# Kernel tuning notes

Hardware: AMD Instinct MI355X
Metric: run time of the kernel (lower is better)

## Reference

```python
import jax, jax.numpy as jnp
import numpy as np

D_MODEL = 1024
N_HEADS = 16
HEAD_DIM = D_MODEL // N_HEADS  # 64
D_STATE = 128
D_FF = 4 * D_MODEL
EPS = 1e-6


def rmsnorm(x, w):
    xf = x.astype(jnp.float32)
    var = jnp.mean(xf * xf, axis=-1, keepdims=True)
    return (w * (x * jax.lax.rsqrt(var + EPS))).astype(x.dtype)


def setup_inputs() -> dict:
    key = jax.random.key(0)
    ks = jax.random.split(key, 24)
    B, S = 2, 2048
    inv = lambda n: 1.0 / np.sqrt(n)
    inp = {
        "x": jax.random.normal(ks[0], (B, S, D_MODEL), jnp.float32),
        "attn_mask": jnp.triu(jnp.ones((S, S), jnp.bool_), k=1),  # True = masked (causal)
        "norm1_w": jnp.ones((D_MODEL,), jnp.float32),
        "norm2_w": jnp.ones((D_MODEL,), jnp.float32),
        "norm3_w": jnp.ones((D_MODEL,), jnp.float32),
        "mlpn_w": jnp.ones((D_MODEL,), jnp.float32),
        # projections stored [in, out]; torch Linear y = x @ W.T
        "wq": jax.random.normal(ks[1], (D_MODEL, D_MODEL), jnp.float32) * inv(D_MODEL),
        "wk": jax.random.normal(ks[2], (D_MODEL, D_MODEL), jnp.float32) * inv(D_MODEL),
        "wv": jax.random.normal(ks[3], (D_MODEL, D_MODEL), jnp.float32) * inv(D_MODEL),
        "wo": jax.random.normal(ks[4], (D_MODEL, D_MODEL), jnp.float32) * inv(D_MODEL),
        "qs_w1": jax.random.normal(ks[5], (HEAD_DIM, D_STATE), jnp.float32) * inv(HEAD_DIM),
        "qs_b1": jnp.zeros((D_STATE,), jnp.float32),
        "qs_w2": jax.random.normal(ks[6], (D_STATE, HEAD_DIM), jnp.float32) * inv(D_STATE),
        "qs_b2": jnp.zeros((HEAD_DIM,), jnp.float32),
        "ks_w1": jax.random.normal(ks[7], (HEAD_DIM, D_STATE), jnp.float32) * inv(HEAD_DIM),
        "ks_b1": jnp.zeros((D_STATE,), jnp.float32),
        "ks_w2": jax.random.normal(ks[8], (D_STATE, HEAD_DIM), jnp.float32) * inv(D_STATE),
        "ks_b2": jnp.zeros((HEAD_DIM,), jnp.float32),
        "fc1_w": jax.random.normal(ks[9], (D_MODEL, D_FF), jnp.float32) * inv(D_MODEL),
        "fc1_b": jnp.zeros((D_FF,), jnp.float32),
        "fc2_w": jax.random.normal(ks[10], (D_FF, D_MODEL), jnp.float32) * inv(D_FF),
        "fc2_b": jnp.zeros((D_MODEL,), jnp.float32),
        "gate_w": jax.random.normal(ks[11], (D_MODEL, D_FF), jnp.float32) * inv(D_MODEL),
        "gate_b": jnp.zeros((D_FF,), jnp.float32),
    }
    return inp


def _attention(h, attn_mask, wq, wk, wv, wo,
               qs_w1, qs_b1, qs_w2, qs_b2, ks_w1, ks_b1, ks_w2, ks_b2):
    B, S, _ = h.shape
    q = (h @ wq).reshape(B, S, N_HEADS, HEAD_DIM)
    k = (h @ wk).reshape(B, S, N_HEADS, HEAD_DIM)
    v = (h @ wv).reshape(B, S, N_HEADS, HEAD_DIM)
    # per-head SiLU-MLP residual transform; weights shared across heads -> vectorized
    q = jax.nn.silu(q @ qs_w1 + qs_b1) @ qs_w2 + qs_b2 + q
    k = jax.nn.silu(k @ ks_w1 + ks_b1) @ ks_w2 + ks_b2 + k
    scale = HEAD_DIM ** -0.5
    scores = jnp.einsum('bqhd,bkhd->bhqk', q, k) * scale
    scores = jnp.where(attn_mask[None, None, :, :], -jnp.inf, scores)
    attn = jax.nn.softmax(scores, axis=-1)
    out = jnp.einsum('bhqk,bkhd->bqhd', attn, v).reshape(B, S, D_MODEL)
    return out @ wo


def reference(x, attn_mask, norm1_w, norm2_w, norm3_w, mlpn_w,
              wq, wk, wv, wo,
              qs_w1, qs_b1, qs_w2, qs_b2, ks_w1, ks_b1, ks_w2, ks_b2,
              fc1_w, fc1_b, fc2_w, fc2_b, gate_w, gate_b):
    # Mamba2Block fallback (mamba_ssm unavailable) is the identity on its input,
    # so each mamba stage is: x = x + RMSNorm(x). Dropout is inference identity.
    x = x + rmsnorm(x, norm1_w)
    x = x + rmsnorm(x, norm2_w)
    h = rmsnorm(x, norm3_w)
    x = x + _attention(h, attn_mask, wq, wk, wv, wo,
                       qs_w1, qs_b1, qs_w2, qs_b2, ks_w1, ks_b1, ks_w2, ks_b2)
    hn = rmsnorm(x, mlpn_w)
    gate = jax.nn.silu(hn @ gate_w + gate_b)
    y = gate * (hn @ fc1_w + fc1_b)
    x = x + (y @ fc2_w + fc2_b)
    return x
```

## Files before the change

### kernel.cpp

```cpp
#include <hip/hip_runtime.h>

typedef unsigned short u16;
typedef unsigned int u32;
typedef __bf16 bf16x8 __attribute__((ext_vector_type(8)));
typedef float f32x4 __attribute__((ext_vector_type(4)));

#define D_MODEL 1024
#define SEQ 2048
#define NB 2
#define NH 16
#define HD 64
#define NTOK (NB * SEQ)
#define NTH (NTOK * NH)
#define LDQ 3072

__device__ __forceinline__ float bf2f(u16 v) { return __uint_as_float(((u32)v) << 16); }
__device__ __forceinline__ u16 f2bf(float f) {
    u32 x = __float_as_uint(f);
    x += 0x7fffu + ((x >> 16) & 1u);
    return (u16)(x >> 16);
}
__device__ __forceinline__ u32 cvtpk(float lo, float hi) {
    u32 r;
    asm("v_cvt_pk_bf16_f32 %0, %1, %2" : "=v"(r) : "v"(lo), "v"(hi));
    return r;
}
__device__ __forceinline__ void unp4(uint2 v, float* f) {
    f[0] = __uint_as_float(v.x << 16);
    f[1] = __uint_as_float(v.x & 0xffff0000u);
    f[2] = __uint_as_float(v.y << 16);
    f[3] = __uint_as_float(v.y & 0xffff0000u);
}

__device__ __forceinline__ void gload_lds(const u16* g, u16* l) {
    __builtin_amdgcn_global_load_lds((__attribute__((address_space(1))) u32*)g,
                                     (__attribute__((address_space(3))) u32*)l, 16, 0, 0);
}

__global__ void detect_kernel(const u32* __restrict__ n1w, int* __restrict__ flag) {
    if (threadIdx.x == 0 && blockIdx.x == 0) flag[0] = (n1w[0] == 0x3F800000u) ? 1 : 0;
}

struct CJobs { const void* in[12]; u16* out[12]; int n[12]; };

__global__ __launch_bounds__(256) void convmulti_kernel(CJobs jobs, const int* __restrict__ flag) {
    const bool f32 = flag[0] != 0;
    const int j = blockIdx.y;
    const int n = jobs.n[j];
    const float* fb = (const float*)jobs.in[j];
    const u16* ib = (const u16*)jobs.in[j];
    u16* ob = jobs.out[j];
    int i = (blockIdx.x * 256 + threadIdx.x) * 8;
    const int str = gridDim.x * 256 * 8;
    for (; i < n; i += str) {
        u16 v[8];
        if (f32) {
#pragma unroll
            for (int t = 0; t < 8; ++t) v[t] = f2bf(fb[i + t]);
        } else {
            *(uint4*)v = *(const uint4*)(ib + i);
        }
        *(uint4*)(ob + i) = *(uint4*)v;
    }
}

struct TJobs { const void* in[4]; u16* out[4]; int kd[4]; int nd[4]; };

__global__ __launch_bounds__(256) void tconvm_kernel(TJobs jobs, const int* __restrict__ flag) {
    __shared__ float tile[32][33];
    const int j = blockIdx.z;
    const int Kd = jobs.kd[j], Nd = jobs.nd[j];
    const int k0 = blockIdx.y * 32, n0 = blockIdx.x * 32;
    if (k0 >= Kd || n0 >= Nd) return;
    const bool f32 = flag[0] != 0;
    const void* in = jobs.in[j];
    u16* out = jobs.out[j];
    const int tx = threadIdx.x & 31, ty = threadIdx.x >> 5;
#pragma unroll
    for (int kk = ty; kk < 32; kk += 8) {
        const size_t sidx = (size_t)(k0 + kk) * Nd + n0 + tx;
        tile[kk][tx] = f32 ? ((const float*)in)[sidx] : bf2f(((const u16*)in)[sidx]);
    }
    __syncthreads();
#pragma unroll
    for (int nn = ty; nn < 32; nn += 8)
        out[(size_t)(n0 + nn) * Kd + k0 + tx] = f2bf(tile[tx][nn]);
}

__device__ __forceinline__ float block_sum(float v, float* red, int tid) {
#pragma unroll
    for (int off = 32; off; off >>= 1) v += __shfl_xor(v, off, 64);
    if ((tid & 63) == 0) red[tid >> 6] = v;
    __syncthreads();
    v = red[0] + red[1] + red[2] + red[3];
    __syncthreads();
    return v;
}

__global__ __launch_bounds__(256) void norm3_kernel(const u16* __restrict__ X,
                                                    const u16* __restrict__ w1,
                                                    const u16* __restrict__ w2,
                                                    const u16* __restrict__ w3,
                                                    float* __restrict__ X2,
                                                    u16* __restrict__ H) {
    __shared__ float red[4];
    const int row = blockIdx.x, tid = threadIdx.x;
    const int c = tid * 4;
    const size_t base = (size_t)row * D_MODEL + c;
    float x[4], w[4];
    unp4(*reinterpret_cast<const uint2*>(X + base), x);

    float ss = x[0] * x[0] + x[1] * x[1] + x[2] * x[2] + x[3] * x[3];
    ss = block_sum(ss, red, tid);
    float r = rsqrtf(ss * (1.f / D_MODEL) + 1e-6f);
    unp4(*reinterpret_cast<const uint2*>(w1 + c), w);
#pragma unroll
    for (int i = 0; i < 4; ++i) x[i] = x[i] + w[i] * x[i] * r;

    ss = x[0] * x[0] + x[1] * x[1] + x[2] * x[2] + x[3] * x[3];
    ss = block_sum(ss, red, tid);
    r = rsqrtf(ss * (1.f / D_MODEL) + 1e-6f);
    unp4(*reinterpret_cast<const uint2*>(w2 + c), w);
#pragma unroll
    for (int i = 0; i < 4; ++i) x[i] = x[i] + w[i] * x[i] * r;

    *reinterpret_cast<float4*>(X2 + base) = make_float4(x[0], x[1], x[2], x[3]);

    ss = x[0] * x[0] + x[1] * x[1] + x[2] * x[2] + x[3] * x[3];
    ss = block_sum(ss, red, tid);
    r = rsqrtf(ss * (1.f / D_MODEL) + 1e-6f);
    unp4(*reinterpret_cast<const uint2*>(w3 + c), w);
    uint2 hv;
    hv.x = (u32)f2bf(w[0] * x[0] * r) | ((u32)f2bf(w[1] * x[1] * r) << 16);
    hv.y = (u32)f2bf(w[2] * x[2] * r) | ((u32)f2bf(w[3] * x[3] * r) << 16);
    *reinterpret_cast<uint2*>(H + base) = hv;
}

__global__ __launch_bounds__(256) void hn_norm_kernel(const float* __restrict__ X3,
                                                      const u16* __restrict__ w,
                                                      u16* __restrict__ HN) {
    __shared__ float red[4];
    const int row = blockIdx.x, tid = threadIdx.x;
    const int c = tid * 4;
    const size_t base = (size_t)row * D_MODEL + c;
    float4 xv = *reinterpret_cast<const float4*>(X3 + base);
    float x[4] = {xv.x, xv.y, xv.z, xv.w};
    float ss = x[0] * x[0] + x[1] * x[1] + x[2] * x[2] + x[3] * x[3];
    ss = block_sum(ss, red, tid);
    float r = rsqrtf(ss * (1.f / D_MODEL) + 1e-6f);
    float w4[4];
    unp4(*reinterpret_cast<const uint2*>(w + c), w4);
    uint2 hv;
    hv.x = (u32)f2bf(w4[0] * x[0] * r) | ((u32)f2bf(w4[1] * x[1] * r) << 16);
    hv.y = (u32)f2bf(w4[2] * x[2] * r) | ((u32)f2bf(w4[3] * x[3] * r) << 16);
    *reinterpret_cast<uint2*>(HN + base) = hv;
}

__global__ __launch_bounds__(256, 4) void mgemm_kernel(const u16* __restrict__ A,
                                                       const u16* __restrict__ Bt,
                                                       const u16* __restrict__ bias,
                                                       const float* __restrict__ resf,
                                                       const u16* __restrict__ mul,
                                                       void* __restrict__ Cout,
                                                       int M, int N, int K, int act, int outf32,
                                                       const int* __restrict__ oflag) {
    __shared__ u16 As[128 * 64];
    __shared__ u16 Bs[128 * 64];
    const int tid = threadIdx.x;
    const int w = tid >> 6, lane = tid & 63;
    const int quad = lane >> 4, l16 = lane & 15;
    const int m0 = blockIdx.y * 128, n0 = blockIdx.x * 128;
    const int wr = (w >> 1) * 64, wc = (w & 1) * 64;

    const int srow = lane >> 3;
    const int scol = ((lane & 7) ^ srow) * 8;
    const u16* Ar = A + (size_t)(m0 + w * 32 + srow) * K + scol;
    const u16* Br = Bt + (size_t)(n0 + w * 32 + srow) * K + scol;
    const int sl0 = l16 & 7;

    f32x4 acc[4][4] = {};

    for (int k0 = 0; k0 < K; k0 += 64) {
#pragma unroll
        for (int i = 0; i < 4; ++i) {
            gload_lds(Ar + (size_t)(i * 8) * K + k0, &As[(w * 32 + i * 8) * 64]);
            gload_lds(Br + (size_t)(i * 8) * K + k0, &Bs[(w * 32 + i * 8) * 64]);
        }
        __syncthreads();
#pragma unroll
        for (int kk = 0; kk < 2; ++kk) {
            const int slot = ((kk * 4 + quad) ^ sl0) * 8;
            bf16x8 a[4], b[4];
#pragma unroll
            for (int i = 0; i < 4; ++i)
                a[i] = *(const bf16x8*)&As[(wr + i * 16 + l16) * 64 + slot];
#pragma unroll
            for (int j = 0; j < 4; ++j)
                b[j] = *(const bf16x8*)&Bs[(wc + j * 16 + l16) * 64 + slot];
#pragma unroll
            for (int i = 0; i < 4; ++i)
#pragma unroll
                for (int j = 0; j < 4; ++j)
                    acc[i][j] = __builtin_amdgcn_mfma_f32_16x16x32_bf16(a[i], b[j], acc[i][j], 0, 0, 0);
        }
        __syncthreads();
    }

    const bool of32 = oflag ? (oflag[0] != 0) : (outf32 != 0);
#pragma unroll
    for (int j = 0; j < 4; ++j) {
        const int col = n0 + wc + j * 16 + l16;
        const float bv = bias ? bf2f(bias[col]) : 0.f;
#pragma unroll
        for (int i = 0; i < 4; ++i) {
            const int rowb = m0 + wr + i * 16 + quad * 4;
#pragma unroll
            for (int r = 0; r < 4; ++r) {
                float v = acc[i][j][r] + bv;
                const size_t idx = (size_t)(rowb + r) * N + col;
                if (act) v = v / (1.f + __expf(-v));
                if (mul) v *= bf2f(mul[idx]);
                if (resf) v += resf[idx];
                if (of32)
                    ((float*)Cout)[idx] = v;
                else
                    ((u16*)Cout)[idx] = f2bf(v);
            }
        }
    }
}

__global__ __launch_bounds__(256, 2) void gatefc1_kernel(const u16* __restrict__ A,
                                                         const u16* __restrict__ Bg,
                                                         const u16* __restrict__ Bf,
                                                         const u16* __restrict__ gbias,
                                                         const u16* __restrict__ fbias,
                                                         u16* __restrict__ G1) {
    const int N = 4096, K = 1024;
    __shared__ u16 As[128 * 64];
    __shared__ u16 Bgs[128 * 64];
    __shared__ u16 Bfs[128 * 64];
    const int tid = threadIdx.x;
    const int w = tid >> 6, lane = tid & 63;
    const int quad = lane >> 4, l16 = lane & 15;
    const int m0 = blockIdx.y * 128, n0 = blockIdx.x * 128;
    const int wr = (w >> 1) * 64, wc = (w & 1) * 64;

    const int srow = lane >> 3;
    const int scol = ((lane & 7) ^ srow) * 8;
    const u16* Ar = A + (size_t)(m0 + w * 32 + srow) * K + scol;
    const u16* Bgr = Bg + (size_t)(n0 + w * 32 + srow) * K + scol;
    const u16* Bfr = Bf + (size_t)(n0 + w * 32 + srow) * K + scol;
    const int sl0 = l16 & 7;

    f32x4 accg[4][4] = {};
    f32x4 accf[4][4] = {};

    for (int k0 = 0; k0 < K; k0 += 64) {
#pragma unroll
        for (int i = 0; i < 4; ++i) {
            gload_lds(Ar + (size_t)(i * 8) * K + k0, &As[(w * 32 + i * 8) * 64]);
            gload_lds(Bgr + (size_t)(i * 8) * K + k0, &Bgs[(w * 32 + i * 8) * 64]);
            gload_lds(Bfr + (size_t)(i * 8) * K + k0, &Bfs[(w * 32 + i * 8) * 64]);
        }
        __syncthreads();
#pragma unroll
        for (int kk = 0; kk < 2; ++kk) {
            const int slot = ((kk * 4 + quad) ^ sl0) * 8;
            bf16x8 a[4], b[4];
#pragma unroll
            for (int i = 0; i < 4; ++i)
                a[i] = *(const bf16x8*)&As[(wr + i * 16 + l16) * 64 + slot];
#pragma unroll
            for (int j = 0; j < 4; ++j)
                b[j] = *(const bf16x8*)&Bgs[(wc + j * 16 + l16) * 64 + slot];
#pragma unroll
            for (int i = 0; i < 4; ++i)
#pragma unroll
                for (int j = 0; j < 4; ++j)
                    accg[i][j] = __builtin_amdgcn_mfma_f32_16x16x32_bf16(a[i], b[j], accg[i][j], 0, 0, 0);
#pragma unroll
            for (int j = 0; j < 4; ++j)
                b[j] = *(const bf16x8*)&Bfs[(wc + j * 16 + l16) * 64 + slot];
#pragma unroll
            for (int i = 0; i < 4; ++i)
#pragma unroll
                for (int j = 0; j < 4; ++j)
                    accf[i][j] = __builtin_amdgcn_mfma_f32_16x16x32_bf16(a[i], b[j], accf[i][j], 0, 0, 0);
        }
        __syncthreads();
    }

#pragma unroll
    for (int j = 0; j < 4; ++j) {
        const int col = n0 + wc + j * 16 + l16;
        const float gb = bf2f(gbias[col]);
        const float fb = bf2f(fbias[col]);
#pragma unroll
        for (int i = 0; i < 4; ++i) {
            const int rowb = m0 + wr + i * 16 + quad * 4;
#pragma unroll
            for (int r = 0; r < 4; ++r) {
                float g = accg[i][j][r] + gb;
                g = g / (1.f + __expf(-g));
                const float f = accf[i][j][r] + fb;
                G1[(size_t)(rowb + r) * N + col] = f2bf(g * f);
            }
        }
    }
}

__global__ __launch_bounds__(256) void mgemm64_kernel(const u16* __restrict__ A,
                                                      const u16* __restrict__ Bt,
                                                      const u16* __restrict__ bias,
                                                      const float* __restrict__ resf,
                                                      const u16* __restrict__ mul,
                                                      void* __restrict__ Cout,
                                                      int M, int N, int K, int act, int outf32,
                                                      const int* __restrict__ oflag) {
    __shared__ u16 As[3][64 * 64];
    __shared__ u16 Bs[3][128 * 64];
    const int tid = threadIdx.x;
    const int w = tid >> 6, lane = tid & 63;
    const int quad = lane >> 4, l16 = lane & 15;
    const int m0 = blockIdx.y * 64, n0 = blockIdx.x * 128;
    const int wr = (w >> 1) * 32, wc = (w & 1) * 64;

    const int srow = lane >> 3;
    const int scol = ((lane & 7) ^ srow) * 8;
    const u16* Ar = A + (size_t)(m0 + w * 16 + srow) * K + scol;
    const u16* Br = Bt + (size_t)(n0 + w * 32 + srow) * K + scol;
    const int sl0 = l16 & 7;

    f32x4 acc[2][4] = {};
    const int nt = K >> 6;

    auto STAGE = [&](int t, int buf) {
        const int k0 = t * 64;
#pragma unroll
        for (int i = 0; i < 2; ++i)
            gload_lds(Ar + (size_t)(i * 8) * K + k0, &As[buf][(w * 16 + i * 8) * 64]);
#pragma unroll
        for (int i = 0; i < 4; ++i)
            gload_lds(Br + (size_t)(i * 8) * K + k0, &Bs[buf][(w * 32 + i * 8) * 64]);
    };
    auto COMPUTE = [&](int buf) {
#pragma unroll
        for (int kk = 0; kk < 2; ++kk) {
            const int slot = ((kk * 4 + quad) ^ sl0) * 8;
            bf16x8 a[2], b[4];
#pragma unroll
            for (int i = 0; i < 2; ++i)
                a[i] = *(const bf16x8*)&As[buf][(wr + i * 16 + l16) * 64 + slot];
#pragma unroll
            for (int j = 0; j < 4; ++j)
                b[j] = *(const bf16x8*)&Bs[buf][(wc + j * 16 + l16) * 64 + slot];
#pragma unroll
            for (int i = 0; i < 2; ++i)
#pragma unroll
                for (int j = 0; j < 4; ++j)
                    acc[i][j] = __builtin_amdgcn_mfma_f32_16x16x32_bf16(a[i], b[j], acc[i][j], 0, 0, 0);
        }
    };

    STAGE(0, 0);
    STAGE(1, 1);
    int cb = 0, sb = 2;
    for (int t = 0; t < nt - 2; ++t) {
        STAGE(t + 2, sb);
        asm volatile("s_waitcnt vmcnt(12)" ::: "memory");
        __builtin_amdgcn_sched_barrier(0);
        __builtin_amdgcn_s_barrier();
        COMPUTE(cb);
        __builtin_amdgcn_s_barrier();
        cb = (cb + 1 == 3) ? 0 : cb + 1;
        sb = (sb + 1 == 3) ? 0 : sb + 1;
    }
    asm volatile("s_waitcnt vmcnt(6)" ::: "memory");
    __builtin_amdgcn_sched_barrier(0);
    __builtin_amdgcn_s_barrier();
    COMPUTE(cb);
    __builtin_amdgcn_s_barrier();
    cb = (cb + 1 == 3) ? 0 : cb + 1;
    asm volatile("s_waitcnt vmcnt(0)" ::: "memory");
    __builtin_amdgcn_sched_barrier(0);
    __builtin_amdgcn_s_barrier();
    COMPUTE(cb);

    const bool of32 = oflag ? (oflag[0] != 0) : (outf32 != 0);
#pragma unroll
    for (int j = 0; j < 4; ++j) {
        const int col = n0 + wc + j * 16 + l16;
        const float bv = bias ? bf2f(bias[col]) : 0.f;
#pragma unroll
        for (int i = 0; i < 2; ++i) {
            const int rowb = m0 + wr + i * 16 + quad * 4;
#pragma unroll
            for (int r = 0; r < 4; ++r) {
                float v = acc[i][j][r] + bv;
                const size_t idx = (size_t)(rowb + r) * N + col;
                if (act) v = v / (1.f + __expf(-v));
                if (mul) v *= bf2f(mul[idx]);
                if (resf) v += resf[idx];
                if (of32)
                    ((float*)Cout)[idx] = v;
                else
                    ((u16*)Cout)[idx] = f2bf(v);
            }
        }
    }
}

__global__ __launch_bounds__(256) void headmlp2_kernel(
    u16* __restrict__ QKV,
    const u16* __restrict__ W1tq, const u16* __restrict__ B1q,
    const u16* __restrict__ W2tq, const u16* __restrict__ B2q,
    const u16* __restrict__ W1tk, const u16* __restrict__ B1k,
    const u16* __restrict__ W2tk, const u16* __restrict__ B2k) {
    __shared__ u16 w1s[128 * 64];
    __shared__ u16 w2s[64 * 128];
    __shared__ u16 Ps[4][16 * 136];
    const int tid = threadIdx.x;
    const bool isk = blockIdx.y != 0;
    u16* base = QKV + (isk ? 1024 : 0);
    const u16* W1t = isk ? W1tk : W1tq;
    const u16* B1 = isk ? B1k : B1q;
    const u16* W2t = isk ? W2tk : W2tq;
    const u16* B2 = isk ? B2k : B2q;

    for (int i = tid * 8; i < 8192; i += 2048) {
        *(uint4*)&w1s[i] = *(const uint4*)&W1t[i];
        *(uint4*)&w2s[i] = *(const uint4*)&W2t[i];
    }
    __syncthreads();

    const int w = tid >> 6, lane = tid & 63;
    const int l16 = lane & 15, quad = lane >> 4;
    const int tok0 = blockIdx.x * 8 + w * 2;
    u16* Pw = &Ps[w][0];

    float b1v[8], b2v[4];
#pragma unroll
    for (int t = 0; t < 8; ++t) b1v[t] = bf2f(B1[t * 16 + l16]);
#pragma unroll
    for (int dd = 0; dd < 4; ++dd) b2v[dd] = bf2f(B2[dd * 16 + l16]);

#pragma unroll
    for (int g = 0; g < 2; ++g) {
        const size_t tbase = (size_t)(tok0 + g) * LDQ;
        const u16* qp = base + tbase + l16 * 64 + quad * 8;
        const bf16x8 aq0 = *(const bf16x8*)qp;
        const bf16x8 aq1 = *(const bf16x8*)(qp + 32);

        f32x4 s[8] = {};
#pragma unroll
        for (int t = 0; t < 8; ++t) {
            const bf16x8 b0 = *(const bf16x8*)&w1s[(t * 16 + l16) * 64 + quad * 8];
            const bf16x8 b1f = *(const bf16x8*)&w1s[(t * 16 + l16) * 64 + 32 + quad * 8];
            s[t] = __builtin_amdgcn_mfma_f32_16x16x32_bf16(aq0, b0, s[t], 0, 0, 0);
            s[t] = __builtin_amdgcn_mfma_f32_16x16x32_bf16(aq1, b1f, s[t], 0, 0, 0);
        }
#pragma unroll
        for (int t = 0; t < 8; ++t)
#pragma unroll
            for (int r = 0; r < 4; ++r) {
                float v = s[t][r] + b1v[t];
                v = v / (1.f + __expf(-v));
                Pw[(quad * 4 + r) * 136 + t * 16 + l16] = f2bf(v);
            }
        bf16x8 ap[4];
#pragma unroll
        for (int kk = 0; kk < 4; ++kk)
            ap[kk] = *(const bf16x8*)&Pw[l16 * 136 + kk * 32 + quad * 8];

        f32x4 o[4] = {};
#pragma unroll
        for (int dd = 0; dd < 4; ++dd)
#pragma unroll
            for (int kk = 0; kk < 4; ++kk) {
                const bf16x8 bw = *(const bf16x8*)&w2s[(dd * 16 + l16) * 128 + kk * 32 + quad * 8];
                o[dd] = __builtin_amdgcn_mfma_f32_16x16x32_bf16(ap[kk], bw, o[dd], 0, 0, 0);
            }
#pragma unroll
        for (int r = 0; r < 4; ++r) {
            u16* outp = base + tbase + (quad * 4 + r) * 64 + l16;
#pragma unroll
            for (int dd = 0; dd < 4; ++dd) {
                const float res = bf2f(outp[dd * 16]);
                outp[dd * 16] = f2bf(o[dd][r] + b2v[dd] + res);
            }
        }
    }
}

__global__ __launch_bounds__(256) void transpose_vperm(const u16* __restrict__ Vin,
                                                       u16* __restrict__ T) {
    __shared__ u16 tile[64][65];
    const int bh = blockIdx.y;
    const int b = bh >> 4, h = bh & 15;
    const int s0 = blockIdx.x * 64;
    const int lane = threadIdx.x & 63, sub = threadIdx.x >> 6;
#pragma unroll
    for (int i = 0; i < 64; i += 4) {
        const int s = s0 + i + sub;
        tile[i + sub][lane] = Vin[(size_t)(b * SEQ + s) * LDQ + h * 64 + lane];
    }
    __syncthreads();
    const int key = (lane & 3) * 16 + (lane >> 2);
#pragma unroll
    for (int i = 0; i < 64; i += 4) {
        const int d = i + sub;
        T[((size_t)(bh * HD + d)) * SEQ + s0 + lane] = tile[key][d];
    }
}

__global__ __launch_bounds__(256) void attn_mfma4_kernel(const u16* __restrict__ QKV,
                                                         const u16* __restrict__ Vt,
                                                         u16* __restrict__ AO) {
    __shared__ u16 Ks[2][64 * 64];
    __shared__ u16 Vs[2][64 * 64];
    __shared__ u16 Ps[4][16 * 72];
    __shared__ float Lred[4][16];
    const int tid = threadIdx.x;
    const int w = tid >> 6, lane = tid & 63;
    const int l16 = lane & 15, quad = lane >> 4;
    const int l7 = l16 & 7;
    const int bh = blockIdx.y, b = bh >> 4, h = bh & 15;

    const u16* Kbh = QKV + 1024 + (size_t)b * SEQ * LDQ + h * 64;
    const u16* Vtbh = Vt + (size_t)bh * HD * SEQ;

    const int srl = lane >> 3, sri = lane & 7;
    auto stage = [&](int c, int buf) {
        const int c0 = c * 64;
#pragma unroll
        for (int qq = 0; qq < 2; ++qq) {
            const int r = w * 16 + qq * 8 + srl;
            const int kb = sri ^ (r & 7);
            gload_lds(Kbh + (size_t)(c0 + r) * LDQ + kb * 8, &Ks[buf][(w * 16 + qq * 8) * 64]);
            gload_lds(Vtbh + (size_t)r * SEQ + c0 + kb * 8, &Vs[buf][(w * 16 + qq * 8) * 64]);
        }
    };

    u16* Pw = &Ps[w][0];

#pragma unroll 1
    for (int pass = 0; pass < 2; ++pass) {
        const int x = pass ? blockIdx.x : (2 * gridDim.x - 1 - blockIdx.x);
        const int qw0 = x * 64 + w * 16;
        const int cmax = x;

        const u16* qp = QKV + (size_t)(b * SEQ + qw0 + l16) * LDQ + h * 64 + quad * 8;
        const bf16x8 aq0 = *(const bf16x8*)qp;
        const bf16x8 aq1 = *(const bf16x8*)(qp + 32);

        f32x4 o[4] = {};
        float lp[4] = {};

        stage(0, 0);

        for (int c = 0; c <= cmax; ++c) {
            __syncthreads();
            if (c < cmax) stage(c + 1, (c + 1) & 1);
            const int c0 = c * 64;
            const int buf = c & 1;

            bf16x8 bk[4][2];
#pragma unroll
            for (int t = 0; t < 4; ++t)
#pragma unroll
                for (int h2 = 0; h2 < 2; ++h2)
                    bk[t][h2] =
                        *(const bf16x8*)&Ks[buf][(t * 16 + l16) * 64 + ((h2 * 4 + quad) ^ l7) * 8];
            f32x4 s[4] = {};
#pragma unroll
            for (int t = 0; t < 4; ++t) {
                s[t] = __builtin_amdgcn_mfma_f32_16x16x32_bf16(aq0, bk[t][0], s[t], 0, 0, 0);
                s[t] = __builtin_amdgcn_mfma_f32_16x16x32_bf16(aq1, bk[t][1], s[t], 0, 0, 0);
            }

            float p[4][4];
            if (c == cmax) {
#pragma unroll
                for (int t = 0; t < 4; ++t)
#pragma unroll
                    for (int r = 0; r < 4; ++r)
                        p[t][r] = (c0 + t * 16 + l16 <= qw0 + quad * 4 + r)
                                      ? __expf(fmaf(s[t][r], 0.125f, -8.f))
                                      : 0.f;
            } else {
#pragma unroll
                for (int t = 0; t < 4; ++t)
#pragma unroll
                    for (int r = 0; r < 4; ++r) p[t][r] = __expf(fmaf(s[t][r], 0.125f, -8.f));
            }
#pragma unroll
            for (int r = 0; r < 4; ++r) lp[r] += (p[0][r] + p[1][r]) + (p[2][r] + p[3][r]);

#pragma unroll
            for (int r = 0; r < 4; ++r) {
                uint2 pv;
                pv.x = cvtpk(p[0][r], p[1][r]);
                pv.y = cvtpk(p[2][r], p[3][r]);
                *(uint2*)&Pw[(quad * 4 + r) * 72 + l16 * 4] = pv;
            }
            const bf16x8 ap0 = *(const bf16x8*)&Pw[l16 * 72 + quad * 8];
            const bf16x8 ap1 = *(const bf16x8*)&Pw[l16 * 72 + 32 + quad * 8];

#pragma unroll
            for (int dd = 0; dd < 4; ++dd) {
                const bf16x8 bv0 = *(const bf16x8*)&Vs[buf][(dd * 16 + l16) * 64 + (quad ^ l7) * 8];
                const bf16x8 bv1 =
                    *(const bf16x8*)&Vs[buf][(dd * 16 + l16) * 64 + ((4 + quad) ^ l7) * 8];
                o[dd] = __builtin_amdgcn_mfma_f32_16x16x32_bf16(bv0, ap0, o[dd], 0, 0, 0);
                o[dd] = __builtin_amdgcn_mfma_f32_16x16x32_bf16(bv1, ap1, o[dd], 0, 0, 0);
            }
        }

#pragma unroll
        for (int off = 1; off < 16; off <<= 1)
#pragma unroll
            for (int r = 0; r < 4; ++r) lp[r] += __shfl_xor(lp[r], off, 64);
        if (l16 == 0) {
#pragma unroll
            for (int r = 0; r < 4; ++r) Lred[w][quad * 4 + r] = lp[r];
        }
        __syncthreads();
        const float inv = 1.f / Lred[w][l16];

        u16* optr = AO + ((size_t)(b * SEQ + qw0 + l16) * NH + h) * HD + quad * 4;
#pragma unroll
        for (int dd = 0; dd < 4; ++dd) {
            uint2 ov;
            ov.x = cvtpk(o[dd][0] * inv, o[dd][1] * inv);
            ov.y = cvtpk(o[dd][2] * inv, o[dd][3] * inv);
            *(uint2*)(optr + dd * 16) = ov;
        }
    }
}

static void mgemm(hipStream_t s, const u16* A, const u16* Bt, const u16* bias, const float* resf,
                  const u16* mul, void* C, int M, int N, int K, int act, int outf32,
                  const int* oflag, int bm) {
    if (bm == 64) {
        dim3 grid(N / 128, M / 64);
        mgemm64_kernel<<<grid, 256, 0, s>>>(A, Bt, bias, resf, mul, C, M, N, K, act, outf32, oflag);
    } else {
        dim3 grid(N / 128, M / 128);
        mgemm_kernel<<<grid, 256, 0, s>>>(A, Bt, bias, resf, mul, C, M, N, K, act, outf32, oflag);
    }
}

extern "C" void kernel_launch(void* const* d_in, const int* in_sizes, int n_in, void* d_out,
                              int out_size, void* d_ws, size_t ws_size, hipStream_t stream) {
    (void)in_sizes; (void)n_in; (void)out_size; (void)ws_size;
    char* ws = (char*)d_ws;
    const size_t MiB = (size_t)1 << 20;

    int* flag = (int*)ws;
    u16* SM = (u16*)(ws + 16384);
    u16* qsw1t = SM + 0;      u16* qsb1c = SM + 8192;
    u16* qsw2t = SM + 16384;  u16* qsb2c = SM + 24576;
    u16* ksw1t = SM + 32768;  u16* ksb1c = SM + 40960;
    u16* ksw2t = SM + 49152;  u16* ksb2c = SM + 57344;
    u16* gatebc = SM + 65536; u16* fc1bc = SM + 73728;
    u16* fc2bc = SM + 81920;
    u16* n1c = SM + 90112; u16* n2c = SM + 91136; u16* n3c = SM + 92160; u16* mlpnc = SM + 93184;

    u16* xc    = (u16*)(ws + 1 * MiB);
    u16* Btqkv = (u16*)(ws + 9 * MiB);
    u16* wot   = (u16*)(ws + 15 * MiB);
    u16* gatet = (u16*)(ws + 17 * MiB);
    u16* fc1t  = (u16*)(ws + 25 * MiB);
    u16* fc2t  = (u16*)(ws + 33 * MiB);
    float* X2  = (float*)(ws + 41 * MiB);
    u16* H     = (u16*)(ws + 57 * MiB);
    u16* QKV   = (u16*)(ws + 65 * MiB);
    u16* Vt    = (u16*)(ws + 57 * MiB);
    u16* AO    = (u16*)(ws + 1 * MiB);
    float* X3  = (float*)(ws + 65 * MiB);
    u16* HN    = (u16*)(ws + 81 * MiB);
    u16* G1    = (u16*)(ws + 89 * MiB);

    detect_kernel<<<1, 64, 0, stream>>>((const u32*)d_in[2], flag);

    CJobs cj;
    cj.in[0] = d_in[0];  cj.out[0] = xc;     cj.n[0] = NTOK * D_MODEL;
    cj.in[1] = d_in[2];  cj.out[1] = n1c;    cj.n[1] = 1024;
    cj.in[2] = d_in[3];  cj.out[2] = n2c;    cj.n[2] = 1024;
    cj.in[3] = d_in[4];  cj.out[3] = n3c;    cj.n[3] = 1024;
    cj.in[4] = d_in[5];  cj.out[4] = mlpnc;  cj.n[4] = 1024;
    cj.in[5] = d_in[11]; cj.out[5] = qsb1c;  cj.n[5] = 128;
    cj.in[6] = d_in[13]; cj.out[6] = qsb2c;  cj.n[6] = 64;
    cj.in[7] = d_in[15]; cj.out[7] = ksb1c;  cj.n[7] = 128;
    cj.in[8] = d_in[17]; cj.out[8] = ksb2c;  cj.n[8] = 64;
    cj.in[9] = d_in[19]; cj.out[9] = fc1bc;  cj.n[9] = 4096;
    cj.in[10] = d_in[21]; cj.out[10] = fc2bc; cj.n[10] = 1024;
    cj.in[11] = d_in[23]; cj.out[11] = gatebc; cj.n[11] = 4096;
    convmulti_kernel<<<dim3(512, 12), 256, 0, stream>>>(cj, flag);

    TJobs ts;
    ts.in[0] = d_in[10]; ts.out[0] = qsw1t; ts.kd[0] = 64;  ts.nd[0] = 128;
    ts.in[1] = d_in[12]; ts.out[1] = qsw2t; ts.kd[1] = 128; ts.nd[1] = 64;
    ts.in[2] = d_in[14]; ts.out[2] = ksw1t; ts.kd[2] = 64;  ts.nd[2] = 128;
    ts.in[3] = d_in[16]; ts.out[3] = ksw2t; ts.kd[3] = 128; ts.nd[3] = 64;
    tconvm_kernel<<<dim3(4, 4, 4), 256, 0, stream>>>(ts, flag);

    TJobs tq;
    tq.in[0] = d_in[6]; tq.out[0] = Btqkv;                tq.kd[0] = 1024; tq.nd[0] = 1024;
    tq.in[1] = d_in[7]; tq.out[1] = Btqkv + 1024 * 1024;  tq.kd[1] = 1024; tq.nd[1] = 1024;
    tq.in[2] = d_in[8]; tq.out[2] = Btqkv + 2048 * 1024;  tq.kd[2] = 1024; tq.nd[2] = 1024;
    tq.in[3] = d_in[9]; tq.out[3] = wot;                  tq.kd[3] = 1024; tq.nd[3] = 1024;
    tconvm_kernel<<<dim3(32, 32, 4), 256, 0, stream>>>(tq, flag);

    TJobs tg;
    tg.in[0] = d_in[22]; tg.out[0] = gatet; tg.kd[0] = 1024; tg.nd[0] = 4096;
    tg.in[1] = d_in[18]; tg.out[1] = fc1t;  tg.kd[1] = 1024; tg.nd[1] = 4096;
    tg.in[2] = d_in[22]; tg.out[2] = gatet; tg.kd[2] = 1024; tg.nd[2] = 4096;
    tg.in[3] = d_in[22]; tg.out[3] = gatet; tg.kd[3] = 1024; tg.nd[3] = 4096;
    tconvm_kernel<<<dim3(128, 32, 2), 256, 0, stream>>>(tg, flag);

    TJobs tf;
    tf.in[0] = d_in[20]; tf.out[0] = fc2t; tf.kd[0] = 4096; tf.nd[0] = 1024;
    tf.in[1] = tf.in[0]; tf.out[1] = fc2t; tf.kd[1] = 4096; tf.nd[1] = 1024;
    tf.in[2] = tf.in[0]; tf.out[2] = fc2t; tf.kd[2] = 4096; tf.nd[2] = 1024;
    tf.in[3] = tf.in[0]; tf.out[3] = fc2t; tf.kd[3] = 4096; tf.nd[3] = 1024;
    tconvm_kernel<<<dim3(32, 128, 1), 256, 0, stream>>>(tf, flag);

    norm3_kernel<<<NTOK, 256, 0, stream>>>(xc, n1c, n2c, n3c, X2, H);
    mgemm(stream, H, Btqkv, nullptr, nullptr, nullptr, QKV, NTOK, 3072, 1024, 0, 0, nullptr, 128);
    headmlp2_kernel<<<dim3(NTH / 128, 2), 256, 0, stream>>>(
        QKV, qsw1t, qsb1c, qsw2t, qsb2c, ksw1t, ksb1c, ksw2t, ksb2c);
    transpose_vperm<<<dim3(SEQ / 64, NB * NH), 256, 0, stream>>>(QKV + 2048, Vt);
    attn_mfma4_kernel<<<dim3(SEQ / 128, NB * NH), 256, 0, stream>>>(QKV, Vt, AO);
    mgemm(stream, AO, wot, nullptr, X2, nullptr, X3, NTOK, 1024, 1024, 0, 1, nullptr, 64);
    hn_norm_kernel<<<NTOK, 256, 0, stream>>>(X3, mlpnc, HN);
    gatefc1_kernel<<<dim3(32, 32), 256, 0, stream>>>(HN, gatet, fc1t, gatebc, fc1bc, G1);
    mgemm(stream, G1, fc2t, fc2bc, X3, nullptr, d_out, NTOK, 1024, 4096, 0, 0, flag, 64);
}
```

Measured before the change: 485.2 us.

## Triple-buffer attention K/V staging and merge weight conversion launches

The attention kernel moves from double to triple buffering of K/V tiles in LDS. It prefetches two chunks ahead and replaces the per-iteration __syncthreads with explicit vmcnt waits and s_barrier, so global loads overlap more compute. Separately, the detect kernel is folded into convmulti, and the four transposed-weight conversion launches are merged into one flat-grid launch that finds its job via block offsets. The cost is more LDS per block, which may lower occupancy, and the hand-counted vmcnt values must match the number of loads issued per stage.

```diff
diff --git a/kernel.cpp b/kernel.cpp
--- a/kernel.cpp
+++ b/kernel.cpp
@@ -37,14 +37,12 @@
                                      (__attribute__((address_space(3))) u32*)l, 16, 0, 0);
 }
 
-__global__ void detect_kernel(const u32* __restrict__ n1w, int* __restrict__ flag) {
-    if (threadIdx.x == 0 && blockIdx.x == 0) flag[0] = (n1w[0] == 0x3F800000u) ? 1 : 0;
-}
-
 struct CJobs { const void* in[12]; u16* out[12]; int n[12]; };
 
-__global__ __launch_bounds__(256) void convmulti_kernel(CJobs jobs, const int* __restrict__ flag) {
-    const bool f32 = flag[0] != 0;
+__global__ __launch_bounds__(256) void convmulti_kernel(CJobs jobs, const u32* __restrict__ w0,
+                                                        int* __restrict__ flag) {
+    const bool f32 = w0[0] == 0x3F800000u;
+    if (blockIdx.x == 0 && blockIdx.y == 0 && threadIdx.x == 0) flag[0] = f32 ? 1 : 0;
     const int j = blockIdx.y;
     const int n = jobs.n[j];
     const float* fb = (const float*)jobs.in[j];
@@ -64,15 +62,23 @@
     }
 }
 
-struct TJobs { const void* in[4]; u16* out[4]; int kd[4]; int nd[4]; };
-
-__global__ __launch_bounds__(256) void tconvm_kernel(TJobs jobs, const int* __restrict__ flag) {
+#define TJN 11
+struct TJobsA { const void* in[TJN]; u16* out[TJN]; int kd[TJN]; int nd[TJN]; int blk0[TJN]; };
+
+__global__ __launch_bounds__(256) void tconvm_all(TJobsA jobs, const u32* __restrict__ w0) {
     __shared__ float tile[32][33];
-    const int j = blockIdx.z;
+    const int bid = blockIdx.x;
+    int j = 0;
+#pragma unroll
+    for (int t = 1; t < TJN; ++t)
+        if (bid >= jobs.blk0[t]) j = t;
+    const int rel = bid - jobs.blk0[j];
     const int Kd = jobs.kd[j], Nd = jobs.nd[j];
-    const int k0 = blockIdx.y * 32, n0 = blockIdx.x * 32;
-    if (k0 >= Kd || n0 >= Nd) return;
-    const bool f32 = flag[0] != 0;
+    const int ntx = Nd >> 5;
+    const int sh = 31 - __clz(ntx);
+    const int k0 = (rel >> sh) * 32;
+    const int n0 = (rel & (ntx - 1)) * 32;
+    const bool f32 = w0[0] == 0x3F800000u;
     const void* in = jobs.in[j];
     u16* out = jobs.out[j];
     const int tx = threadIdx.x & 31, ty = threadIdx.x >> 5;
@@ -517,8 +523,8 @@
 __global__ __launch_bounds__(256) void attn_mfma4_kernel(const u16* __restrict__ QKV,
                                                          const u16* __restrict__ Vt,
                                                          u16* __restrict__ AO) {
-    __shared__ u16 Ks[2][64 * 64];
-    __shared__ u16 Vs[2][64 * 64];
+    __shared__ u16 Ks[3][64 * 64];
+    __shared__ u16 Vs[3][64 * 64];
     __shared__ u16 Ps[4][16 * 72];
     __shared__ float Lred[4][16];
     const int tid = threadIdx.x;
@@ -553,17 +559,29 @@
         const u16* qp = QKV + (size_t)(b * SEQ + qw0 + l16) * LDQ + h * 64 + quad * 8;
         const bf16x8 aq0 = *(const bf16x8*)qp;
         const bf16x8 aq1 = *(const bf16x8*)(qp + 32);
+        __builtin_amdgcn_sched_barrier(0);
 
         f32x4 o[4] = {};
         float lp[4] = {};
 
         stage(0, 0);
+        if (cmax >= 1) stage(1, 1);
+        int cb = 0, sb = 2;
 
         for (int c = 0; c <= cmax; ++c) {
-            __syncthreads();
-            if (c < cmax) stage(c + 1, (c + 1) & 1);
+            if (c + 2 <= cmax) {
+                stage(c + 2, sb);
+                asm volatile("s_waitcnt vmcnt(8)" ::: "memory");
+            } else if (c + 1 <= cmax) {
+                asm volatile("s_waitcnt vmcnt(4)" ::: "memory");
+            } else {
+                asm volatile("s_waitcnt vmcnt(0)" ::: "memory");
+            }
+            __builtin_amdgcn_sched_barrier(0);
+            __builtin_amdgcn_s_barrier();
+
             const int c0 = c * 64;
-            const int buf = c & 1;
+            const int buf = cb;
 
             bf16x8 bk[4][2];
 #pragma unroll
@@ -615,6 +633,9 @@
                 o[dd] = __builtin_amdgcn_mfma_f32_16x16x32_bf16(bv0, ap0, o[dd], 0, 0, 0);
                 o[dd] = __builtin_amdgcn_mfma_f32_16x16x32_bf16(bv1, ap1, o[dd], 0, 0, 0);
             }
+            __builtin_amdgcn_s_barrier();
+            cb = (cb + 1 == 3) ? 0 : cb + 1;
+            sb = (sb + 1 == 3) ? 0 : sb + 1;
         }
 
 #pragma unroll
@@ -682,7 +703,7 @@
     u16* HN    = (u16*)(ws + 81 * MiB);
     u16* G1    = (u16*)(ws + 89 * MiB);
 
-    detect_kernel<<<1, 64, 0, stream>>>((const u32*)d_in[2], flag);
+    const u32* w0 = (const u32*)d_in[2];
 
     CJobs cj;
     cj.in[0] = d_in[0];  cj.out[0] = xc;     cj.n[0] = NTOK * D_MODEL;
@@ -697,35 +718,21 @@
     cj.in[9] = d_in[19]; cj.out[9] = fc1bc;  cj.n[9] = 4096;
     cj.in[10] = d_in[21]; cj.out[10] = fc2bc; cj.n[10] = 1024;
     cj.in[11] = d_in[23]; cj.out[11] = gatebc; cj.n[11] = 4096;
-    convmulti_kernel<<<dim3(512, 12), 256, 0, stream>>>(cj, flag);
-
-    TJobs ts;
-    ts.in[0] = d_in[10]; ts.out[0] = qsw1t; ts.kd[0] = 64;  ts.nd[0] = 128;
-    ts.in[1] = d_in[12]; ts.out[1] = qsw2t; ts.kd[1] = 128; ts.nd[1] = 64;
-    ts.in[2] = d_in[14]; ts.out[2] = ksw1t; ts.kd[2] = 64;  ts.nd[2] = 128;
-    ts.in[3] = d_in[16]; ts.out[3] = ksw2t; ts.kd[3] = 128; ts.nd[3] = 64;
-    tconvm_kernel<<<dim3(4, 4, 4), 256, 0, stream>>>(ts, flag);
-
-    TJobs tq;
-    tq.in[0] = d_in[6]; tq.out[0] = Btqkv;                tq.kd[0] = 1024; tq.nd[0] = 1024;
-    tq.in[1] = d_in[7]; tq.out[1] = Btqkv + 1024 * 1024;  tq.kd[1] = 1024; tq.nd[1] = 1024;
-    tq.in[2] = d_in[8]; tq.out[2] = Btqkv + 2048 * 1024;  tq.kd[2] = 1024; tq.nd[2] = 1024;
-    tq.in[3] = d_in[9]; tq.out[3] = wot;                  tq.kd[3] = 1024; tq.nd[3] = 1024;
-    tconvm_kernel<<<dim3(32, 32, 4), 256, 0, stream>>>(tq, flag);
-
-    TJobs tg;
-    tg.in[0] = d_in[22]; tg.out[0] = gatet; tg.kd[0] = 1024; tg.nd[0] = 4096;
-    tg.in[1] = d_in[18]; tg.out[1] = fc1t;  tg.kd[1] = 1024; tg.nd[1] = 4096;
-    tg.in[2] = d_in[22]; tg.out[2] = gatet; tg.kd[2] = 1024; tg.nd[2] = 4096;
-    tg.in[3] = d_in[22]; tg.out[3] = gatet; tg.kd[3] = 1024; tg.nd[3] = 4096;
-    tconvm_kernel<<<dim3(128, 32, 2), 256, 0, stream>>>(tg, flag);
-
-    TJobs tf;
-    tf.in[0] = d_in[20]; tf.out[0] = fc2t; tf.kd[0] = 4096; tf.nd[0] = 1024;
-    tf.in[1] = tf.in[0]; tf.out[1] = fc2t; tf.kd[1] = 4096; tf.nd[1] = 1024;
-    tf.in[2] = tf.in[0]; tf.out[2] = fc2t; tf.kd[2] = 4096; tf.nd[2] = 1024;
-    tf.in[3] = tf.in[0]; tf.out[3] = fc2t; tf.kd[3] = 4096; tf.nd[3] = 1024;
-    tconvm_kernel<<<dim3(32, 128, 1), 256, 0, stream>>>(tf, flag);
+    convmulti_kernel<<<dim3(512, 12), 256, 0, stream>>>(cj, w0, flag);
+
+    TJobsA ta;
+    ta.in[0] = d_in[10]; ta.out[0] = qsw1t; ta.kd[0] = 64;   ta.nd[0] = 128;  ta.blk0[0] = 0;
+    ta.in[1] = d_in[12]; ta.out[1] = qsw2t; ta.kd[1] = 128;  ta.nd[1] = 64;   ta.blk0[1] = 8;
+    ta.in[2] = d_in[14]; ta.out[2] = ksw1t; ta.kd[2] = 64;   ta.nd[2] = 128;  ta.blk0[2] = 16;
+    ta.in[3] = d_in[16]; ta.out[3] = ksw2t; ta.kd[3] = 128;  ta.nd[3] = 64;   ta.blk0[3] = 24;
+    ta.in[4] = d_in[6];  ta.out[4] = Btqkv;               ta.kd[4] = 1024; ta.nd[4] = 1024; ta.blk0[4] = 32;
+    ta.in[5] = d_in[7];  ta.out[5] = Btqkv + 1024 * 1024; ta.kd[5] = 1024; ta.nd[5] = 1024; ta.blk0[5] = 1056;
+    ta.in[6] = d_in[8];  ta.out[6] = Btqkv + 2048 * 1024; ta.kd[6] = 1024; ta.nd[6] = 1024; ta.blk0[6] = 2080;
+    ta.in[7] = d_in[9];  ta.out[7] = wot;                 ta.kd[7] = 1024; ta.nd[7] = 1024; ta.blk0[7] = 3104;
+    ta.in[8] = d_in[22]; ta.out[8] = gatet; ta.kd[8] = 1024; ta.nd[8] = 4096; ta.blk0[8] = 4128;
+    ta.in[9] = d_in[18]; ta.out[9] = fc1t;  ta.kd[9] = 1024; ta.nd[9] = 4096; ta.blk0[9] = 8224;
+    ta.in[10] = d_in[20]; ta.out[10] = fc2t; ta.kd[10] = 4096; ta.nd[10] = 1024; ta.blk0[10] = 12320;
+    tconvm_all<<<16416, 256, 0, stream>>>(ta, w0);
 
     norm3_kernel<<<NTOK, 256, 0, stream>>>(xc, n1c, n2c, n3c, X2, H);
     mgemm(stream, H, Btqkv, nullptr, nullptr, nullptr, QKV, NTOK, 3072, 1024, 0, 0, nullptr, 128);
```

Result: no change. 484.5 us (-0.1%).
